# Performance work log

Measured on AMD Instinct MI355X. Metric: run time of the kernel, lower is better.

Reference implementation:

```python
import jax, jax.numpy as jnp
import numpy as np

B = 1024          # batch_size from init
TEMP = 0.5        # temperature buffer
EPS_NORM = 1e-12  # F.normalize eps
EPS_COS = 1e-8    # F.cosine_similarity eps


def setup_inputs() -> dict:
    key = jax.random.key(0)
    k1, k2 = jax.random.split(key)
    emb_i = jax.random.normal(k1, (B, 128, 128), dtype=jnp.float32)
    emb_j = jax.random.normal(k2, (B, 128, 128), dtype=jnp.float32)
    return {"emb_i": emb_i, "emb_j": emb_j}


def reference(emb_i, emb_j):
    # F.normalize(x, dim=1): L2-normalize over the m axis of [B, m, n]
    def norm_dim1(x):
        n = jnp.sqrt(jnp.sum(x * x, axis=1, keepdims=True))
        return x / jnp.maximum(n, EPS_NORM)

    z_i = norm_dim1(emb_i)
    z_j = norm_dim1(emb_j)
    reps = jnp.concatenate([z_i, z_j], axis=0)        # [2B, m, n]
    flat = reps.reshape(2 * B, -1)                    # [2B, D]

    # cosine similarity of flattened vectors == matmul of re-normalized rows
    rn = flat / jnp.maximum(
        jnp.sqrt(jnp.sum(flat * flat, axis=1, keepdims=True)), EPS_COS)
    sim = rn @ rn.T                                   # [2B, 2B]

    sim_ij = jnp.diagonal(sim, offset=B)              # [B]
    sim_ji = jnp.diagonal(sim, offset=-B)             # [B]
    positives = jnp.concatenate([sim_ij, sim_ji], axis=0)  # [2B]

    negatives_mask = 1.0 - jnp.eye(2 * B, dtype=sim.dtype)
    nominator = jnp.exp(positives / TEMP)
    denominator = jnp.sum(negatives_mask * jnp.exp(sim / TEMP), axis=1)
    loss_partial = -jnp.log(nominator / denominator)
    return jnp.sum(loss_partial) / (2 * B)
```

## Files before the change

kernel.cpp:

```cpp
#include <hip/hip_runtime.h>
#include <hip/hip_bf16.h>
#include <math.h>

#define B_SZ   1024
#define NROW   2048
#define D_K    16384
#define TEMP_INV 2.0f
#define SPLIT  8
#define KSEG   (D_K / SPLIT)
#define NTILE  16
#define NPAIR  136

typedef float f32x4 __attribute__((ext_vector_type(4)));
typedef long  i64;

typedef __attribute__((address_space(1))) unsigned int GU32;
typedef __attribute__((address_space(3))) unsigned int LU32;

__device__ __forceinline__ void async16(const void* g, void* l) {
  __builtin_amdgcn_global_load_lds((GU32*)(g), (LU32*)(l), 16, 0, 0);
}

__global__ __launch_bounds__(256) void norm_kernel(
    const float* __restrict__ emb_i, const float* __restrict__ emb_j,
    unsigned char* __restrict__ rn, float* __restrict__ sim,
    float* __restrict__ rsum)
{
  const int b = blockIdx.x;
  const int t = threadIdx.x;
  const int c = t & 31;
  const int g = t >> 5;

  {
    f32x4* sz = (f32x4*)sim + (size_t)b * 512 + t * 2;
    sz[0] = (f32x4){0.f, 0.f, 0.f, 0.f};
    sz[1] = (f32x4){0.f, 0.f, 0.f, 0.f};
  }
  if (b == 0) {
    for (int k = t; k < NROW; k += 256) rsum[k] = 0.f;
  }

  const float* src = (b < B_SZ) ? (emb_i + (size_t)b * D_K)
                                : (emb_j + (size_t)(b - B_SZ) * D_K);

  f32x4 vals[16];
  f32x4 ss = (f32x4){0.f, 0.f, 0.f, 0.f};
#pragma unroll
  for (int mm = 0; mm < 16; ++mm) {
    f32x4 v = *(const f32x4*)(src + (size_t)(g * 16 + mm) * 128 + c * 4);
    vals[mm] = v;
    ss += v * v;
  }

  __shared__ f32x4 part[8][32];
  part[g][c] = ss;
  __syncthreads();
  f32x4 css = part[0][c];
#pragma unroll
  for (int gg = 1; gg < 8; ++gg) css += part[gg][c];

  f32x4 mcn, colz2;
#pragma unroll
  for (int k = 0; k < 4; ++k) {
    mcn[k] = fmaxf(sqrtf(css[k]), 1e-12f);
    colz2[k] = css[k] / (mcn[k] * mcn[k]);
  }
  float s = colz2[0] + colz2[1] + colz2[2] + colz2[3];
#pragma unroll
  for (int off = 1; off < 64; off <<= 1) s += __shfl_xor(s, off);
  const float rowss = 0.5f * s;
  const float rowfac = fmaxf(sqrtf(rowss), 1e-8f);

  f32x4 scale;
#pragma unroll
  for (int k = 0; k < 4; ++k) scale[k] = 1.f / (mcn[k] * rowfac);

  unsigned char* dst = rn + (size_t)b * D_K;
#pragma unroll
  for (int mm = 0; mm < 16; ++mm) {
    f32x4 sv = vals[mm] * scale;
    int p = 0;
    p = __builtin_amdgcn_cvt_pk_fp8_f32(sv[0], sv[1], p, false);
    p = __builtin_amdgcn_cvt_pk_fp8_f32(sv[2], sv[3], p, true);
    *(int*)(dst + (size_t)(g * 16 + mm) * 128 + c * 4) = p;
  }
}

__global__ __launch_bounds__(256) void gemm_sim_kernel(
    const unsigned char* __restrict__ rn, float* __restrict__ sim)
{
  int idx = blockIdx.y, tI = 0, rem = NTILE;
  while (idx >= rem) { idx -= rem; --rem; ++tI; }
  const int tJ = tI + idx;
  const bool diag = (tI == tJ);

  const int kBase = blockIdx.x * KSEG;
  const int t    = threadIdx.x;
  const int lane = t & 63;
  const int wave = t >> 6;
  const int wm = wave >> 1, wn = wave & 1;
  const int quad = lane >> 4, col = lane & 15;

  __shared__ __align__(16) unsigned char As[128 * 32];
  __shared__ __align__(16) unsigned char Bs[128 * 32];

  const unsigned char* aG = rn + (size_t)(tI * 128 + (t >> 1)) * D_K + kBase + (t & 1) * 16;
  const unsigned char* bG = rn + (size_t)(tJ * 128 + (t >> 1)) * D_K + kBase + (t & 1) * 16;
  unsigned char* aL = &As[t * 16];
  unsigned char* bL = &Bs[t * 16];

  f32x4 acc[4][4];
#pragma unroll
  for (int mi = 0; mi < 4; ++mi)
#pragma unroll
    for (int ni = 0; ni < 4; ++ni)
      acc[mi][ni] = (f32x4){0.f, 0.f, 0.f, 0.f};

  const unsigned char* aLr = &As[(wm * 64 + col) * 32 + quad * 8];
  const unsigned char* bLr = &Bs[(wn * 64 + col) * 32 + quad * 8];

  for (int k0 = 0; k0 < KSEG; k0 += 32) {
    __syncthreads();
    async16(aG + k0, aL);
    async16(bG + k0, bL);
    __syncthreads();

    i64 af[4], bf[4];
#pragma unroll
    for (int mi = 0; mi < 4; ++mi) af[mi] = *(const i64*)(aLr + mi * 16 * 32);
#pragma unroll
    for (int ni = 0; ni < 4; ++ni) bf[ni] = *(const i64*)(bLr + ni * 16 * 32);
#pragma unroll
    for (int mi = 0; mi < 4; ++mi)
#pragma unroll
      for (int ni = 0; ni < 4; ++ni)
        acc[mi][ni] = __builtin_amdgcn_mfma_f32_16x16x32_fp8_fp8(
            af[mi], bf[ni], acc[mi][ni], 0, 0, 0);
  }

  const int iB = tI * 128 + wm * 64;
  const int jB = tJ * 128 + wn * 64;
#pragma unroll
  for (int mi = 0; mi < 4; ++mi) {
#pragma unroll
    for (int reg = 0; reg < 4; ++reg) {
      const int i = iB + mi * 16 + quad * 4 + reg;
#pragma unroll
      for (int ni = 0; ni < 4; ++ni) {
        const int j = jB + ni * 16 + col;
        if (!diag || j >= i)
          atomicAdd(&sim[(size_t)i * NROW + j], acc[mi][ni][reg]);
      }
    }
  }
}

__global__ __launch_bounds__(256) void loss_tile_kernel(
    const float* __restrict__ sim, float* __restrict__ rsum)
{
  int idx = blockIdx.x, tI = 0, rem = NTILE;
  while (idx >= rem) { idx -= rem; --rem; ++tI; }
  const int tJ = tI + idx;
  const bool diag = (tI == tJ);

  const int t   = threadIdx.x;
  const int w   = t >> 6;
  const int l   = t & 63;
  const int hf  = l >> 5;
  const int sub = l & 31;
  const int jb  = tJ * 128 + sub * 4;

  float ca[4] = {0.f, 0.f, 0.f, 0.f};

#pragma unroll
  for (int step = 0; step < 16; ++step) {
    const int r  = w * 32 + step * 2 + hf;
    const int gi = tI * 128 + r;
    f32x4 v = *(const f32x4*)(sim + (size_t)gi * NROW + jb);
    float e[4];
#pragma unroll
    for (int k = 0; k < 4; ++k) {
      e[k] = __expf(TEMP_INV * v[k]);
      if (diag && (jb + k <= gi)) e[k] = 0.f;
      ca[k] += e[k];
    }
    float rp = e[0] + e[1] + e[2] + e[3];
#pragma unroll
    for (int off = 1; off < 32; off <<= 1) rp += __shfl_xor(rp, off);
    if (sub == 0) atomicAdd(&rsum[gi], rp);
  }

  __shared__ float colacc[8][128];
#pragma unroll
  for (int k = 0; k < 4; ++k) colacc[w * 2 + hf][sub * 4 + k] = ca[k];
  __syncthreads();
  if (t < 128) {
    float s = 0.f;
#pragma unroll
    for (int q = 0; q < 8; ++q) s += colacc[q][t];
    atomicAdd(&rsum[tJ * 128 + t], s);
  }
}

__global__ __launch_bounds__(256) void final_kernel(
    const float* __restrict__ sim, const float* __restrict__ rsum,
    float* __restrict__ out)
{
  const int t = threadIdx.x;
  float s = 0.f;
  for (int i = t; i < NROW; i += 256) {
    const int jp = (i < B_SZ) ? i + B_SZ : i - B_SZ;
    const float pos = (jp >= i) ? sim[(size_t)i * NROW + jp]
                                : sim[(size_t)jp * NROW + i];
    s += logf(rsum[i]) - TEMP_INV * pos;
  }
#pragma unroll
  for (int off = 1; off < 64; off <<= 1) s += __shfl_xor(s, off);
  __shared__ float r[4];
  if ((t & 63) == 0) r[t >> 6] = s;
  __syncthreads();
  if (t == 0) out[0] = (r[0] + r[1] + r[2] + r[3]) * (1.0f / NROW);
}

extern "C" void kernel_launch(void* const* d_in, const int* in_sizes, int n_in,
                              void* d_out, int out_size, void* d_ws, size_t ws_size,
                              hipStream_t stream) {
  const float* emb_i = (const float*)d_in[0];
  const float* emb_j = (const float*)d_in[1];
  float* out = (float*)d_out;

  char* ws = (char*)d_ws;
  unsigned char* rn = (unsigned char*)ws;
  float* sim  = (float*)(ws + (size_t)NROW * D_K);
  float* rsum = sim + (size_t)NROW * NROW;

  norm_kernel<<<dim3(NROW), dim3(256), 0, stream>>>(emb_i, emb_j, rn, sim, rsum);
  gemm_sim_kernel<<<dim3(SPLIT, NPAIR), dim3(256), 0, stream>>>(rn, sim);
  loss_tile_kernel<<<dim3(NPAIR), dim3(256), 0, stream>>>(sim, rsum);
  final_kernel<<<1, 256, 0, stream>>>(sim, rsum, out);
}
```

Baseline: 288.6 us.

## Fuse final reduction into loss kernel, widen norm blocks, double K-step in GEMM

Several changes at once. The final loss reduction moves into the last loss_tile block using an atomic completion counter, which removes one kernel launch. norm_kernel now runs 512 threads per row with half the registers per thread, and FP8 values are pre-scaled by 16 to make better use of the FP8 range, with the exp temperature compensated by 1/256. The GEMM loads two 32-wide K slices per barrier pair, halving the number of synchronizations. The added risks are reliance on the counter and threadfence ordering, and possible FP8 saturation if a scaled element exceeds the format range.

```diff
diff --git a/kernel.cpp b/kernel.cpp
--- a/kernel.cpp
+++ b/kernel.cpp
@@ -5,11 +5,11 @@
 #define B_SZ   1024
 #define NROW   2048
 #define D_K    16384
-#define TEMP_INV 2.0f
 #define SPLIT  8
 #define KSEG   (D_K / SPLIT)
 #define NTILE  16
 #define NPAIR  136
+#define TEMP_SIM (2.0f / 256.0f)
 
 typedef float f32x4 __attribute__((ext_vector_type(4)));
 typedef long  i64;
@@ -21,43 +21,40 @@
   __builtin_amdgcn_global_load_lds((GU32*)(g), (LU32*)(l), 16, 0, 0);
 }
 
-__global__ __launch_bounds__(256) void norm_kernel(
+__global__ __launch_bounds__(512) void norm_kernel(
     const float* __restrict__ emb_i, const float* __restrict__ emb_j,
     unsigned char* __restrict__ rn, float* __restrict__ sim,
-    float* __restrict__ rsum)
+    float* __restrict__ rsum, unsigned int* __restrict__ cnt)
 {
   const int b = blockIdx.x;
   const int t = threadIdx.x;
   const int c = t & 31;
   const int g = t >> 5;
 
-  {
-    f32x4* sz = (f32x4*)sim + (size_t)b * 512 + t * 2;
-    sz[0] = (f32x4){0.f, 0.f, 0.f, 0.f};
-    sz[1] = (f32x4){0.f, 0.f, 0.f, 0.f};
-  }
+  ((f32x4*)sim)[(size_t)b * 512 + t] = (f32x4){0.f, 0.f, 0.f, 0.f};
   if (b == 0) {
-    for (int k = t; k < NROW; k += 256) rsum[k] = 0.f;
+    for (int k = t; k < NROW; k += 512) rsum[k] = 0.f;
+    if (t == 0) *cnt = 0u;
   }
 
   const float* src = (b < B_SZ) ? (emb_i + (size_t)b * D_K)
                                 : (emb_j + (size_t)(b - B_SZ) * D_K);
 
-  f32x4 vals[16];
+  f32x4 vals[8];
   f32x4 ss = (f32x4){0.f, 0.f, 0.f, 0.f};
 #pragma unroll
-  for (int mm = 0; mm < 16; ++mm) {
-    f32x4 v = *(const f32x4*)(src + (size_t)(g * 16 + mm) * 128 + c * 4);
+  for (int mm = 0; mm < 8; ++mm) {
+    f32x4 v = *(const f32x4*)(src + (size_t)(g * 8 + mm) * 128 + c * 4);
     vals[mm] = v;
     ss += v * v;
   }
 
-  __shared__ f32x4 part[8][32];
+  __shared__ f32x4 part[16][32];
   part[g][c] = ss;
   __syncthreads();
   f32x4 css = part[0][c];
 #pragma unroll
-  for (int gg = 1; gg < 8; ++gg) css += part[gg][c];
+  for (int gg = 1; gg < 16; ++gg) css += part[gg][c];
 
   f32x4 mcn, colz2;
 #pragma unroll
@@ -68,21 +65,20 @@
   float s = colz2[0] + colz2[1] + colz2[2] + colz2[3];
 #pragma unroll
   for (int off = 1; off < 64; off <<= 1) s += __shfl_xor(s, off);
-  const float rowss = 0.5f * s;
-  const float rowfac = fmaxf(sqrtf(rowss), 1e-8f);
+  const float rowfac = fmaxf(sqrtf(0.5f * s), 1e-8f);
 
   f32x4 scale;
 #pragma unroll
-  for (int k = 0; k < 4; ++k) scale[k] = 1.f / (mcn[k] * rowfac);
+  for (int k = 0; k < 4; ++k) scale[k] = 16.0f / (mcn[k] * rowfac);
 
   unsigned char* dst = rn + (size_t)b * D_K;
 #pragma unroll
-  for (int mm = 0; mm < 16; ++mm) {
+  for (int mm = 0; mm < 8; ++mm) {
     f32x4 sv = vals[mm] * scale;
     int p = 0;
     p = __builtin_amdgcn_cvt_pk_fp8_f32(sv[0], sv[1], p, false);
     p = __builtin_amdgcn_cvt_pk_fp8_f32(sv[2], sv[3], p, true);
-    *(int*)(dst + (size_t)(g * 16 + mm) * 128 + c * 4) = p;
+    *(int*)(dst + (size_t)(g * 8 + mm) * 128 + c * 4) = p;
   }
 }
 
@@ -101,13 +97,15 @@
   const int wm = wave >> 1, wn = wave & 1;
   const int quad = lane >> 4, col = lane & 15;
 
-  __shared__ __align__(16) unsigned char As[128 * 32];
-  __shared__ __align__(16) unsigned char Bs[128 * 32];
+  __shared__ __align__(16) unsigned char As[2][128 * 32];
+  __shared__ __align__(16) unsigned char Bs[2][128 * 32];
 
   const unsigned char* aG = rn + (size_t)(tI * 128 + (t >> 1)) * D_K + kBase + (t & 1) * 16;
   const unsigned char* bG = rn + (size_t)(tJ * 128 + (t >> 1)) * D_K + kBase + (t & 1) * 16;
-  unsigned char* aL = &As[t * 16];
-  unsigned char* bL = &Bs[t * 16];
+  unsigned char* aL0 = &As[0][t * 16];
+  unsigned char* aL1 = &As[1][t * 16];
+  unsigned char* bL0 = &Bs[0][t * 16];
+  unsigned char* bL1 = &Bs[1][t * 16];
 
   f32x4 acc[4][4];
 #pragma unroll
@@ -116,26 +114,31 @@
     for (int ni = 0; ni < 4; ++ni)
       acc[mi][ni] = (f32x4){0.f, 0.f, 0.f, 0.f};
 
-  const unsigned char* aLr = &As[(wm * 64 + col) * 32 + quad * 8];
-  const unsigned char* bLr = &Bs[(wn * 64 + col) * 32 + quad * 8];
-
-  for (int k0 = 0; k0 < KSEG; k0 += 32) {
+  const int aOff = (wm * 64 + col) * 32 + quad * 8;
+  const int bOff = (wn * 64 + col) * 32 + quad * 8;
+
+  for (int k0 = 0; k0 < KSEG; k0 += 64) {
     __syncthreads();
-    async16(aG + k0, aL);
-    async16(bG + k0, bL);
+    async16(aG + k0,      aL0);
+    async16(aG + k0 + 32, aL1);
+    async16(bG + k0,      bL0);
+    async16(bG + k0 + 32, bL1);
     __syncthreads();
 
-    i64 af[4], bf[4];
-#pragma unroll
-    for (int mi = 0; mi < 4; ++mi) af[mi] = *(const i64*)(aLr + mi * 16 * 32);
-#pragma unroll
-    for (int ni = 0; ni < 4; ++ni) bf[ni] = *(const i64*)(bLr + ni * 16 * 32);
-#pragma unroll
-    for (int mi = 0; mi < 4; ++mi)
-#pragma unroll
-      for (int ni = 0; ni < 4; ++ni)
-        acc[mi][ni] = __builtin_amdgcn_mfma_f32_16x16x32_fp8_fp8(
-            af[mi], bf[ni], acc[mi][ni], 0, 0, 0);
+#pragma unroll
+    for (int h = 0; h < 2; ++h) {
+      i64 af[4], bf[4];
+#pragma unroll
+      for (int mi = 0; mi < 4; ++mi) af[mi] = *(const i64*)(&As[h][aOff + mi * 16 * 32]);
+#pragma unroll
+      for (int ni = 0; ni < 4; ++ni) bf[ni] = *(const i64*)(&Bs[h][bOff + ni * 16 * 32]);
+#pragma unroll
+      for (int mi = 0; mi < 4; ++mi)
+#pragma unroll
+        for (int ni = 0; ni < 4; ++ni)
+          acc[mi][ni] = __builtin_amdgcn_mfma_f32_16x16x32_fp8_fp8(
+              af[mi], bf[ni], acc[mi][ni], 0, 0, 0);
+    }
   }
 
   const int iB = tI * 128 + wm * 64;
@@ -156,7 +159,8 @@
 }
 
 __global__ __launch_bounds__(256) void loss_tile_kernel(
-    const float* __restrict__ sim, float* __restrict__ rsum)
+    const float* __restrict__ sim, float* __restrict__ rsum,
+    unsigned int* __restrict__ cnt, float* __restrict__ out)
 {
   int idx = blockIdx.x, tI = 0, rem = NTILE;
   while (idx >= rem) { idx -= rem; --rem; ++tI; }
@@ -180,7 +184,7 @@
     float e[4];
 #pragma unroll
     for (int k = 0; k < 4; ++k) {
-      e[k] = __expf(TEMP_INV * v[k]);
+      e[k] = __expf(TEMP_SIM * v[k]);
       if (diag && (jb + k <= gi)) e[k] = 0.f;
       ca[k] += e[k];
     }
@@ -200,19 +204,23 @@
     for (int q = 0; q < 8; ++q) s += colacc[q][t];
     atomicAdd(&rsum[tJ * 128 + t], s);
   }
-}
-
-__global__ __launch_bounds__(256) void final_kernel(
-    const float* __restrict__ sim, const float* __restrict__ rsum,
-    float* __restrict__ out)
-{
-  const int t = threadIdx.x;
+
+  __syncthreads();
+  __shared__ bool last;
+  if (t == 0) {
+    __threadfence();
+    last = (atomicAdd(cnt, 1u) == NPAIR - 1);
+  }
+  __syncthreads();
+  if (!last) return;
+
   float s = 0.f;
   for (int i = t; i < NROW; i += 256) {
     const int jp = (i < B_SZ) ? i + B_SZ : i - B_SZ;
     const float pos = (jp >= i) ? sim[(size_t)i * NROW + jp]
                                 : sim[(size_t)jp * NROW + i];
-    s += logf(rsum[i]) - TEMP_INV * pos;
+    const float rs = atomicAdd(&rsum[i], 0.f);
+    s += logf(rs) - TEMP_SIM * pos;
   }
 #pragma unroll
   for (int off = 1; off < 64; off <<= 1) s += __shfl_xor(s, off);
@@ -233,9 +241,9 @@
   unsigned char* rn = (unsigned char*)ws;
   float* sim  = (float*)(ws + (size_t)NROW * D_K);
   float* rsum = sim + (size_t)NROW * NROW;
-
-  norm_kernel<<<dim3(NROW), dim3(256), 0, stream>>>(emb_i, emb_j, rn, sim, rsum);
+  unsigned int* cnt = (unsigned int*)(rsum + NROW);
+
+  norm_kernel<<<dim3(NROW), dim3(512), 0, stream>>>(emb_i, emb_j, rn, sim, rsum, cnt);
   gemm_sim_kernel<<<dim3(SPLIT, NPAIR), dim3(256), 0, stream>>>(rn, sim);
-  loss_tile_kernel<<<dim3(NPAIR), dim3(256), 0, stream>>>(sim, rsum);
-  final_kernel<<<1, 256, 0, stream>>>(sim, rsum, out);
-}
+  loss_tile_kernel<<<dim3(NPAIR), dim3(256), 0, stream>>>(sim, rsum, cnt, out);
+}
```

Measured after the change: 286.4 us. About the same (-0.8%).
